# Optimization experiments

Measured on AMD Instinct MI355X. Metric: run time of the kernel, lower is better.

Reference implementation:

```python
import jax, jax.numpy as jnp
import numpy as np

D_QKV = 64

def setup_inputs() -> dict:
    key = jax.random.key(0)
    k1, k2, k3, k4 = jax.random.split(key, 4)
    B, T, D = 4, 2048, 1024
    x = jax.random.normal(k1, (B, T, D), dtype=jnp.float32)
    Wq = jax.random.normal(k2, (D, D_QKV), dtype=jnp.float32) * (D ** -0.5)
    Wk = jax.random.normal(k3, (D, D_QKV), dtype=jnp.float32) * (D ** -0.5)
    Wv = jax.random.normal(k4, (D, D_QKV), dtype=jnp.float32) * (D ** -0.5)
    return {"x": x, "Wq": Wq, "Wk": Wk, "Wv": Wv}

def reference(x, Wq, Wk, Wv):
    # x: [B, T, D]; single-head causal attention with head dim d_qkv
    T = x.shape[1]
    q = jnp.einsum("btd,de->bte", x, Wq)  # [B, T, d]
    k = jnp.einsum("btd,de->bte", x, Wk)
    v = jnp.einsum("btd,de->bte", x, Wv)
    scores = jnp.einsum("bqe,bke->bqk", q, k) / (D_QKV ** 0.5)  # [B, T, T]
    causal = jnp.tril(jnp.ones((T, T), dtype=bool))
    scores = jnp.where(causal, scores, -jnp.inf)
    attn = jax.nn.softmax(scores, axis=2)
    return jnp.einsum("bqk,bke->bqe", attn, v)  # [B, T, d]
```

## Files before the change

kernel.cpp:

```cpp
#include <hip/hip_runtime.h>
#include <hip/hip_bf16.h>
#include <math.h>

typedef __hip_bfloat16 bf16;
typedef __bf16 bf16x8 __attribute__((ext_vector_type(8)));
typedef float f32x4 __attribute__((ext_vector_type(4)));
typedef unsigned short u16x8 __attribute__((ext_vector_type(8)));

#define B_SZ   4
#define T_SEQ  2048
#define D_IN   1024
#define D_QKV  64
#define BT     (B_SZ * T_SEQ)
#define PSTR   72
#define TOTW   2112
#define ANB    512

#define GLD_LDS(gp, lp) __builtin_amdgcn_global_load_lds(                     \
    (const __attribute__((address_space(1))) void*)(gp),                      \
    (__attribute__((address_space(3))) void*)(lp), 16, 0, 0)

#define VMCNT0 asm volatile("s_waitcnt vmcnt(0)" ::: "memory")
#define VMCNT1 asm volatile("s_waitcnt vmcnt(1)" ::: "memory")
#define VMCNT2 asm volatile("s_waitcnt vmcnt(2)" ::: "memory")
#define VMCNT4 asm volatile("s_waitcnt vmcnt(4)" ::: "memory")

__global__ __launch_bounds__(256) void wt_prep(
    const float* __restrict__ Wq, const float* __restrict__ Wk,
    const float* __restrict__ Wv, bf16* __restrict__ wt)
{
    __shared__ float ws[64 * 65];
    const int bx = blockIdx.x;
    const int m  = bx >> 4;
    const int k0 = (bx & 15) << 6;
    const float* W = (m == 0) ? Wq : (m == 1) ? Wk : Wv;
    const int tid = threadIdx.x;
    #pragma unroll
    for (int i = 0; i < 16; ++i) {
        const int idx = i * 256 + tid;
        const int kk = idx >> 6, nn = idx & 63;
        ws[kk * 65 + nn] = W[(size_t)(k0 + kk) * D_QKV + nn];
    }
    __syncthreads();
    const int n = tid >> 2, kq = (tid & 3) << 4;
    bf16 tmp[16];
    #pragma unroll
    for (int j = 0; j < 16; ++j)
        tmp[j] = __float2bfloat16(ws[(kq + j) * 65 + n]);
    uint4* dst = (uint4*)(wt + (size_t)(m * 64 + n) * D_IN + k0 + kq);
    dst[0] = ((uint4*)tmp)[0];
    dst[1] = ((uint4*)tmp)[1];
}

__global__ __launch_bounds__(256) void qkv_proj_mfma(
    const float* __restrict__ x, const bf16* __restrict__ wt,
    bf16* __restrict__ qb, bf16* __restrict__ kb, bf16* __restrict__ vt)
{
    __shared__ uint4 As[4][256];
    __shared__ uint4 Bs[2][1536];

    const int tid  = threadIdx.x;
    const int wave = tid >> 6;
    const int lane = tid & 63;
    const int col  = lane & 15;
    const int quad = lane >> 4;
    const int m0   = blockIdx.x * 16;

    f32x4 acc[3];
    #pragma unroll
    for (int i = 0; i < 3; ++i) acc[i] = (f32x4){0.f, 0.f, 0.f, 0.f};

    auto stage_A = [&](int it, int buf) {
        const int k0 = it * 64;
        const int s = wave;
        const int c = s * 64 + lane;
        const int r = c >> 4;
        const int ccl = ((c & 15) - r) & 15;
        const float* g = x + (size_t)(m0 + r) * D_IN + k0 + ccl * 4;
        GLD_LDS(g, &As[buf][s * 64]);
    };
    auto stage_B = [&](int it, int buf) {
        const int k0 = it * 64;
        #pragma unroll
        for (int j = 0; j < 6; ++j) {
            const int bs = wave + j * 4;
            const int c = bs * 64 + lane;
            const int n = c >> 3;
            const int ccl = ((c & 7) - n) & 7;
            const bf16* g = wt + (size_t)n * D_IN + k0 + ccl * 8;
            GLD_LDS(g, &Bs[buf][bs * 64]);
        }
    };

    stage_B(0, 0);
    stage_A(0, 0);
    stage_A(1, 1);
    stage_A(2, 2);

    const int r = col;
    #pragma unroll 1
    for (int it = 0; it < 16; ++it) {
        if (it == 0)       VMCNT2;
        else if (it < 14)  VMCNT1;
        else               VMCNT0;
        __builtin_amdgcn_s_barrier();

        if (it + 1 < 16) stage_B(it + 1, (it + 1) & 1);
        if (it + 3 < 16) stage_A(it + 3, (it + 3) & 3);

        const float4* Ac = (const float4*)As[it & 3];
        const uint4*  Bc = Bs[it & 1];
        #pragma unroll
        for (int s = 0; s < 2; ++s) {
            const int ca = s * 8 + quad * 2;
            const float4 a0 = Ac[r * 16 + ((ca + r) & 15)];
            const float4 a1 = Ac[r * 16 + ((ca + 1 + r) & 15)];
            const bf16x8 af = (bf16x8){(__bf16)a0.x, (__bf16)a0.y, (__bf16)a0.z, (__bf16)a0.w,
                                       (__bf16)a1.x, (__bf16)a1.y, (__bf16)a1.z, (__bf16)a1.w};
            #pragma unroll
            for (int i = 0; i < 3; ++i) {
                const int n = wave * 48 + i * 16 + col;
                const bf16x8 bfr = __builtin_bit_cast(bf16x8,
                    Bc[n * 8 + ((s * 4 + quad + n) & 7)]);
                acc[i] = __builtin_amdgcn_mfma_f32_16x16x32_bf16(af, bfr, acc[i], 0, 0, 0);
            }
        }
    }

    const int bb = m0 >> 11;
    const int tl = m0 & (T_SEQ - 1);
    #pragma unroll
    for (int i = 0; i < 3; ++i) {
        const int n = wave * 48 + i * 16 + col;
        #pragma unroll
        for (int rr = 0; rr < 4; ++rr) {
            const int row = m0 + quad * 4 + rr;
            const bf16 vq = __float2bfloat16(acc[i][rr]);
            if (n < 64)       qb[(size_t)row * D_QKV + n] = vq;
            else if (n < 128) kb[(size_t)row * D_QKV + (n - 64)] = vq;
            else              vt[(size_t)bb * D_QKV * T_SEQ + (size_t)(n - 128) * T_SEQ
                                 + (tl + quad * 4 + rr)] = vq;
        }
    }
}

__global__ __launch_bounds__(256) void attn_kernel(
    const bf16* __restrict__ qb, const bf16* __restrict__ kb,
    const bf16* __restrict__ vt, float* __restrict__ Op, float* __restrict__ lp)
{
    __shared__ uint4 Ks[3][512];
    __shared__ uint4 Vs[3][512];
    __shared__ unsigned short plds[4 * 16 * PSTR];

    const int tid  = threadIdx.x;
    const int wave = tid >> 6;
    const int lane = tid & 63;
    const int col  = lane & 15;
    const int quad = lane >> 4;
    const int bx   = blockIdx.x;

    const int lo = (bx * 33) >> 3;
    const int hi = ((bx + 1) * 33) >> 3;
    const int items = hi - lo;

    int b = lo / 528;
    int rres = lo - b * 528;
    int t = (int)((sqrtf(8.f * (float)rres + 1.f) - 1.f) * 0.5f);
    while ((t + 1) * (t + 2) / 2 <= rres) ++t;
    while (t * (t + 1) / 2 > rres) --t;
    int c = rres - t * (t + 1) / 2;

    unsigned short* pl = plds + wave * 16 * PSTR;
    const u16x8* p8 = (const u16x8*)pl;

    auto stage = [&](int sb, int sc, int buf) {
        const bf16* kbp = kb + (size_t)sb * T_SEQ * D_QKV;
        const bf16* vtp = vt + (size_t)sb * D_QKV * T_SEQ;
        const int kb0 = sc * 64;
        #pragma unroll
        for (int j = 0; j < 4; ++j) {
            const int s = wave + j * 4;
            if (s < 8) {
                const int ch = s * 64 + lane;
                const int key = ch >> 3;
                const int ccl = ((ch & 7) - key) & 7;
                const bf16* g = kbp + (size_t)(kb0 + key) * D_QKV + ccl * 8;
                GLD_LDS(g, &Ks[buf][s * 64]);
            } else {
                const int vs = s - 8;
                const int ch = vs * 64 + lane;
                const int d = ch >> 3;
                const int ccl = ((ch & 7) - d) & 7;
                const bf16* g = vtp + (size_t)d * T_SEQ + kb0 + ccl * 8;
                GLD_LDS(g, &Vs[buf][vs * 64]);
            }
        }
    };

    auto adv = [](int& ab, int& at, int& ac) {
        if (++ac > at) { ac = 0; if (++at == 32) { at = 0; ++ab; } }
    };

    stage(b, c, 0);
    int bn = b, tn = t, cn = c;
    adv(bn, tn, cn);
    if (items > 1) stage(bn, cn, 1);

    bf16x8 aq0, aq1;
    f32x4 o[4];
    float ls[4];
    int segw = lo;

    #pragma unroll 1
    for (int i = 0; i < items; ++i) {
        const bool segstart = (i == 0 || c == 0);

        if (i == 0) {
            if (items > 1) VMCNT4; else VMCNT0;
        } else if (c == 0 || i + 1 >= items) {
            VMCNT0;
        } else {
            VMCNT4;
        }
        __builtin_amdgcn_s_barrier();

        if (i + 2 < items) {
            int b2 = bn, t2 = tn, c2 = cn;
            adv(b2, t2, c2);
            stage(b2, c2, (i + 2) % 3);
        }

        if (segstart) {
            const uint4* q4 = (const uint4*)(qb + (size_t)b * T_SEQ * D_QKV);
            const int qrow = t * 64 + wave * 16 + col;
            aq0 = __builtin_bit_cast(bf16x8, q4[qrow * 8 + quad]);
            aq1 = __builtin_bit_cast(bf16x8, q4[qrow * 8 + 4 + quad]);
            #pragma unroll
            for (int dt = 0; dt < 4; ++dt) o[dt] = (f32x4){0.f, 0.f, 0.f, 0.f};
            #pragma unroll
            for (int rr = 0; rr < 4; ++rr) ls[rr] = 0.f;
            segw = lo + i;
        }

        const uint4* Kc = Ks[i % 3];
        const uint4* Vc = Vs[i % 3];

        f32x4 sc4[4];
        #pragma unroll
        for (int nt2 = 0; nt2 < 4; ++nt2) {
            const int kp = nt2 * 16 + col;
            const bf16x8 bk0 = __builtin_bit_cast(bf16x8, Kc[kp * 8 + ((quad + kp) & 7)]);
            const bf16x8 bk1 = __builtin_bit_cast(bf16x8, Kc[kp * 8 + ((4 + quad + kp) & 7)]);
            sc4[nt2] = (f32x4){0.f, 0.f, 0.f, 0.f};
            sc4[nt2] = __builtin_amdgcn_mfma_f32_16x16x32_bf16(aq0, bk0, sc4[nt2], 0, 0, 0);
            sc4[nt2] = __builtin_amdgcn_mfma_f32_16x16x32_bf16(aq1, bk1, sc4[nt2], 0, 0, 0);
        }

        if (c == t) {
            #pragma unroll
            for (int nt2 = 0; nt2 < 4; ++nt2) {
                const int kp = c * 64 + nt2 * 16 + col;
                #pragma unroll
                for (int rr = 0; rr < 4; ++rr)
                    if (kp > t * 64 + wave * 16 + quad * 4 + rr) sc4[nt2][rr] = -INFINITY;
            }
        }

        #pragma unroll
        for (int nt2 = 0; nt2 < 4; ++nt2) {
            #pragma unroll
            for (int rr = 0; rr < 4; ++rr) {
                const float pv = __expf(sc4[nt2][rr] * 0.125f);
                ls[rr] += pv;
                pl[(quad * 4 + rr) * PSTR + nt2 * 16 + col] =
                    __builtin_bit_cast(unsigned short, __float2bfloat16(pv));
            }
        }

        const bf16x8 pa0 = __builtin_bit_cast(bf16x8, p8[col * 9 + quad]);
        const bf16x8 pa1 = __builtin_bit_cast(bf16x8, p8[col * 9 + 4 + quad]);

        #pragma unroll
        for (int dt = 0; dt < 4; ++dt) {
            const int dp = dt * 16 + col;
            const bf16x8 bv0 = __builtin_bit_cast(bf16x8, Vc[dp * 8 + ((quad + dp) & 7)]);
            const bf16x8 bv1 = __builtin_bit_cast(bf16x8, Vc[dp * 8 + ((4 + quad + dp) & 7)]);
            o[dt] = __builtin_amdgcn_mfma_f32_16x16x32_bf16(pa0, bv0, o[dt], 0, 0, 0);
            o[dt] = __builtin_amdgcn_mfma_f32_16x16x32_bf16(pa1, bv1, o[dt], 0, 0, 0);
        }

        if (c == t || i == items - 1) {
            float lr[4];
            #pragma unroll
            for (int rr = 0; rr < 4; ++rr) {
                lr[rr] = ls[rr];
                #pragma unroll
                for (int msk = 1; msk < 16; msk <<= 1)
                    lr[rr] += __shfl_xor(lr[rr], msk);
            }
            const int pbase = segw * 64 + wave * 16;
            #pragma unroll
            for (int dt = 0; dt < 4; ++dt)
                #pragma unroll
                for (int rr = 0; rr < 4; ++rr)
                    Op[(size_t)(pbase + quad * 4 + rr) * D_QKV + dt * 16 + col] = o[dt][rr];
            if (col == 0) {
                #pragma unroll
                for (int rr = 0; rr < 4; ++rr)
                    lp[pbase + quad * 4 + rr] = lr[rr];
            }
        }

        b = bn; t = tn; c = cn;
        adv(bn, tn, cn);
    }
}

__global__ __launch_bounds__(256) void combine_attn(
    const float* __restrict__ Op, const float* __restrict__ lp,
    float* __restrict__ out)
{
    const int idx = blockIdx.x * 256 + threadIdx.x;
    const int qg = idx >> 6, d = idx & 63;
    const int g = qg >> 6, qq = qg & 63;
    const int b = g >> 5, t = g & 31;
    const int W0 = b * 528 + t * (t + 1) / 2;
    float s = 0.f, l = 0.f;
    int prevown = (8 * (W0 - 1) + 7) / 33;
    #pragma unroll 1
    for (int c = 0; c <= t; ++c) {
        const int w = W0 + c;
        const int own = (8 * w + 7) / 33;
        if (c == 0 || own != prevown) {
            s += Op[(size_t)(w * 64 + qq) * D_QKV + d];
            l += lp[w * 64 + qq];
        }
        prevown = own;
    }
    out[(size_t)qg * D_QKV + d] = s / l;
}

extern "C" void kernel_launch(void* const* d_in, const int* in_sizes, int n_in,
                              void* d_out, int out_size, void* d_ws, size_t ws_size,
                              hipStream_t stream) {
    const float* x  = (const float*)d_in[0];
    const float* Wq = (const float*)d_in[1];
    const float* Wk = (const float*)d_in[2];
    const float* Wv = (const float*)d_in[3];
    float* out = (float*)d_out;

    char* ws = (char*)d_ws;
    bf16*  qb = (bf16*)(ws);
    bf16*  kb = (bf16*)(ws + (1u << 20));
    bf16*  vt = (bf16*)(ws + (2u << 20));
    bf16*  wt = (bf16*)(ws + (3u << 20));
    float* Op = (float*)(ws + (4u << 20));
    float* lp = (float*)(ws + (40u << 20));

    wt_prep<<<48, 256, 0, stream>>>(Wq, Wk, Wv, wt);
    qkv_proj_mfma<<<512, 256, 0, stream>>>(x, wt, qb, kb, vt);
    attn_kernel<<<ANB, 256, 0, stream>>>(qb, kb, vt, Op, lp);
    combine_attn<<<2048, 256, 0, stream>>>(Op, lp, out);
}
```

Before: 110.2 us.

## Replace balanced split-KV attention and combine pass with one block per query tile

Drops the load-balanced work split, where 512 blocks each took a contiguous run of (batch, query tile, key chunk) items and wrote partial outputs, along with the separate combine kernel. Each of 128 blocks now owns one query tile, walks all its causal key chunks, and writes the normalized output directly. This removes the partial-result traffic, the final reduction pass and one kernel launch. In exchange it launches far fewer blocks than the GPU has compute units, and the work per block is very uneven: the last tile handles 32 chunks while the first handles one.

```diff
diff --git a/kernel.cpp b/kernel.cpp
--- a/kernel.cpp
+++ b/kernel.cpp
@@ -13,8 +13,6 @@
 #define D_QKV  64
 #define BT     (B_SZ * T_SEQ)
 #define PSTR   72
-#define TOTW   2112
-#define ANB    512
 
 #define GLD_LDS(gp, lp) __builtin_amdgcn_global_load_lds(                     \
     (const __attribute__((address_space(1))) void*)(gp),                      \
@@ -146,7 +144,7 @@
 
 __global__ __launch_bounds__(256) void attn_kernel(
     const bf16* __restrict__ qb, const bf16* __restrict__ kb,
-    const bf16* __restrict__ vt, float* __restrict__ Op, float* __restrict__ lp)
+    const bf16* __restrict__ vt, float* __restrict__ out)
 {
     __shared__ uint4 Ks[3][512];
     __shared__ uint4 Vs[3][512];
@@ -158,25 +156,30 @@
     const int col  = lane & 15;
     const int quad = lane >> 4;
     const int bx   = blockIdx.x;
-
-    const int lo = (bx * 33) >> 3;
-    const int hi = ((bx + 1) * 33) >> 3;
-    const int items = hi - lo;
-
-    int b = lo / 528;
-    int rres = lo - b * 528;
-    int t = (int)((sqrtf(8.f * (float)rres + 1.f) - 1.f) * 0.5f);
-    while ((t + 1) * (t + 2) / 2 <= rres) ++t;
-    while (t * (t + 1) / 2 > rres) --t;
-    int c = rres - t * (t + 1) / 2;
+    const int b    = bx >> 5;
+    const int t    = bx & 31;
+    const int nch  = t + 1;
+
+    const bf16* kbp = kb + (size_t)b * T_SEQ * D_QKV;
+    const bf16* vtp = vt + (size_t)b * D_QKV * T_SEQ;
+    const uint4* q4 = (const uint4*)(qb + (size_t)b * T_SEQ * D_QKV);
+
+    const int qrow = t * 64 + wave * 16 + col;
+    const bf16x8 aq0 = __builtin_bit_cast(bf16x8, q4[qrow * 8 + quad]);
+    const bf16x8 aq1 = __builtin_bit_cast(bf16x8, q4[qrow * 8 + 4 + quad]);
+
+    f32x4 o[4];
+    float ls[4];
+    #pragma unroll
+    for (int dt = 0; dt < 4; ++dt) o[dt] = (f32x4){0.f, 0.f, 0.f, 0.f};
+    #pragma unroll
+    for (int rr = 0; rr < 4; ++rr) ls[rr] = 0.f;
 
     unsigned short* pl = plds + wave * 16 * PSTR;
     const u16x8* p8 = (const u16x8*)pl;
 
-    auto stage = [&](int sb, int sc, int buf) {
-        const bf16* kbp = kb + (size_t)sb * T_SEQ * D_QKV;
-        const bf16* vtp = vt + (size_t)sb * D_QKV * T_SEQ;
-        const int kb0 = sc * 64;
+    auto stage = [&](int c, int buf) {
+        const int kb0 = c * 64;
         #pragma unroll
         for (int j = 0; j < 4; ++j) {
             const int s = wave + j * 4;
@@ -197,53 +200,17 @@
         }
     };
 
-    auto adv = [](int& ab, int& at, int& ac) {
-        if (++ac > at) { ac = 0; if (++at == 32) { at = 0; ++ab; } }
-    };
-
-    stage(b, c, 0);
-    int bn = b, tn = t, cn = c;
-    adv(bn, tn, cn);
-    if (items > 1) stage(bn, cn, 1);
-
-    bf16x8 aq0, aq1;
-    f32x4 o[4];
-    float ls[4];
-    int segw = lo;
+    stage(0, 0);
+    if (nch > 1) stage(1, 1);
 
     #pragma unroll 1
-    for (int i = 0; i < items; ++i) {
-        const bool segstart = (i == 0 || c == 0);
-
-        if (i == 0) {
-            if (items > 1) VMCNT4; else VMCNT0;
-        } else if (c == 0 || i + 1 >= items) {
-            VMCNT0;
-        } else {
-            VMCNT4;
-        }
+    for (int c = 0; c < nch; ++c) {
+        if (c + 1 < nch) VMCNT4; else VMCNT0;
         __builtin_amdgcn_s_barrier();
-
-        if (i + 2 < items) {
-            int b2 = bn, t2 = tn, c2 = cn;
-            adv(b2, t2, c2);
-            stage(b2, c2, (i + 2) % 3);
-        }
-
-        if (segstart) {
-            const uint4* q4 = (const uint4*)(qb + (size_t)b * T_SEQ * D_QKV);
-            const int qrow = t * 64 + wave * 16 + col;
-            aq0 = __builtin_bit_cast(bf16x8, q4[qrow * 8 + quad]);
-            aq1 = __builtin_bit_cast(bf16x8, q4[qrow * 8 + 4 + quad]);
-            #pragma unroll
-            for (int dt = 0; dt < 4; ++dt) o[dt] = (f32x4){0.f, 0.f, 0.f, 0.f};
-            #pragma unroll
-            for (int rr = 0; rr < 4; ++rr) ls[rr] = 0.f;
-            segw = lo + i;
-        }
-
-        const uint4* Kc = Ks[i % 3];
-        const uint4* Vc = Vs[i % 3];
+        if (c + 2 < nch) stage(c + 2, (c + 2) % 3);
+
+        const uint4* Kc = Ks[c % 3];
+        const uint4* Vc = Vs[c % 3];
 
         f32x4 sc4[4];
         #pragma unroll
@@ -288,56 +255,25 @@
             o[dt] = __builtin_amdgcn_mfma_f32_16x16x32_bf16(pa0, bv0, o[dt], 0, 0, 0);
             o[dt] = __builtin_amdgcn_mfma_f32_16x16x32_bf16(pa1, bv1, o[dt], 0, 0, 0);
         }
-
-        if (c == t || i == items - 1) {
-            float lr[4];
-            #pragma unroll
-            for (int rr = 0; rr < 4; ++rr) {
-                lr[rr] = ls[rr];
-                #pragma unroll
-                for (int msk = 1; msk < 16; msk <<= 1)
-                    lr[rr] += __shfl_xor(lr[rr], msk);
-            }
-            const int pbase = segw * 64 + wave * 16;
-            #pragma unroll
-            for (int dt = 0; dt < 4; ++dt)
-                #pragma unroll
-                for (int rr = 0; rr < 4; ++rr)
-                    Op[(size_t)(pbase + quad * 4 + rr) * D_QKV + dt * 16 + col] = o[dt][rr];
-            if (col == 0) {
-                #pragma unroll
-                for (int rr = 0; rr < 4; ++rr)
-                    lp[pbase + quad * 4 + rr] = lr[rr];
-            }
-        }
-
-        b = bn; t = tn; c = cn;
-        adv(bn, tn, cn);
-    }
-}
-
-__global__ __launch_bounds__(256) void combine_attn(
-    const float* __restrict__ Op, const float* __restrict__ lp,
-    float* __restrict__ out)
-{
-    const int idx = blockIdx.x * 256 + threadIdx.x;
-    const int qg = idx >> 6, d = idx & 63;
-    const int g = qg >> 6, qq = qg & 63;
-    const int b = g >> 5, t = g & 31;
-    const int W0 = b * 528 + t * (t + 1) / 2;
-    float s = 0.f, l = 0.f;
-    int prevown = (8 * (W0 - 1) + 7) / 33;
-    #pragma unroll 1
-    for (int c = 0; c <= t; ++c) {
-        const int w = W0 + c;
-        const int own = (8 * w + 7) / 33;
-        if (c == 0 || own != prevown) {
-            s += Op[(size_t)(w * 64 + qq) * D_QKV + d];
-            l += lp[w * 64 + qq];
-        }
-        prevown = own;
-    }
-    out[(size_t)qg * D_QKV + d] = s / l;
+    }
+
+    float lr[4];
+    #pragma unroll
+    for (int rr = 0; rr < 4; ++rr) {
+        lr[rr] = ls[rr];
+        #pragma unroll
+        for (int msk = 1; msk < 16; msk <<= 1)
+            lr[rr] += __shfl_xor(lr[rr], msk);
+    }
+
+    const int rowb = b * T_SEQ + t * 64 + wave * 16 + quad * 4;
+    #pragma unroll
+    for (int rr = 0; rr < 4; ++rr) {
+        const float rden = 1.f / lr[rr];
+        #pragma unroll
+        for (int dt = 0; dt < 4; ++dt)
+            out[(size_t)(rowb + rr) * D_QKV + dt * 16 + col] = o[dt][rr] * rden;
+    }
 }
 
 extern "C" void kernel_launch(void* const* d_in, const int* in_sizes, int n_in,
@@ -354,11 +290,8 @@
     bf16*  kb = (bf16*)(ws + (1u << 20));
     bf16*  vt = (bf16*)(ws + (2u << 20));
     bf16*  wt = (bf16*)(ws + (3u << 20));
-    float* Op = (float*)(ws + (4u << 20));
-    float* lp = (float*)(ws + (40u << 20));
 
     wt_prep<<<48, 256, 0, stream>>>(Wq, Wk, Wv, wt);
     qkv_proj_mfma<<<512, 256, 0, stream>>>(x, wt, qb, kb, vt);
-    attn_kernel<<<ANB, 256, 0, stream>>>(qb, kb, vt, Op, lp);
-    combine_attn<<<2048, 256, 0, stream>>>(Op, lp, out);
-}
+    attn_kernel<<<128, 256, 0, stream>>>(qb, kb, vt, out);
+}
```

Result: slower. 119.2 us (+8.2%).
